# Kernel optimization log

Hardware: AMD Instinct MI355X
Metric: run time of the kernel (lower is better)

## Reference

```python
import jax, jax.numpy as jnp
import numpy as np

N_HEADS = 16

def setup_inputs() -> dict:
    key = jax.random.key(0)
    ks = jax.random.split(key, 5)
    B, T, C = 4, 2048, 1024
    x = jax.random.normal(ks[0], (B, T, C), dtype=jnp.float32)
    w_qkv = jax.random.normal(ks[1], (C, 3 * C), dtype=jnp.float32) * (C ** -0.5)
    b_qkv = jnp.zeros((3 * C,), dtype=jnp.float32)
    w_proj = jax.random.normal(ks[2], (C, C), dtype=jnp.float32) * (C ** -0.5)
    b_proj = jnp.zeros((C,), dtype=jnp.float32)
    return {"x": x, "w_qkv": w_qkv, "b_qkv": b_qkv, "w_proj": w_proj, "b_proj": b_proj}


def reference(x, w_qkv, b_qkv, w_proj, b_proj):
    B, T, C = x.shape
    H = N_HEADS
    hd = C // H
    scale = hd ** -0.5
    qkv = x @ w_qkv + b_qkv                      # [B,T,3C]
    q, k, v = jnp.split(qkv, 3, axis=-1)         # each [B,T,C]
    # -> [B,H,T,hd]
    q = q.reshape(B, T, H, hd).transpose(0, 2, 1, 3)
    k = k.reshape(B, T, H, hd).transpose(0, 2, 1, 3)
    v = v.reshape(B, T, H, hd).transpose(0, 2, 1, 3)
    attn = jnp.einsum("bhqd,bhkd->bhqk", q, k) * scale
    causal = jnp.tril(jnp.ones((T, T), dtype=bool))
    attn = jnp.where(causal, attn, -jnp.inf)
    attn = jax.nn.softmax(attn, axis=-1)         # dropout p=0 in eval/reference
    out = jnp.einsum("bhqk,bhkd->bhqd", attn, v)
    out = out.transpose(0, 2, 1, 3).reshape(B, T, C)
    return out @ w_proj + b_proj
```

## Files before the change

### kernel.cpp

```cpp
#include <hip/hip_runtime.h>
#include <hip/hip_bf16.h>


typedef float f32x4 __attribute__((ext_vector_type(4)));
typedef float f32x16 __attribute__((ext_vector_type(16)));
typedef __bf16 bf16x8 __attribute__((ext_vector_type(8)));
typedef short short8v __attribute__((ext_vector_type(8)));
typedef unsigned int u32x4 __attribute__((ext_vector_type(4)));

__device__ __forceinline__ unsigned short f2bf(float f) {
  __hip_bfloat16 h = __float2bfloat16(f);
  return __builtin_bit_cast(unsigned short, h);
}

__device__ __forceinline__ void glds16(const void* g, void* l) {
  __builtin_amdgcn_global_load_lds((const __attribute__((address_space(1))) void*)g,
                                   (__attribute__((address_space(3))) void*)l, 16, 0, 0);
}

__global__ void cvt_f32_bf16_kernel(const float* __restrict__ in,
                                    unsigned short* __restrict__ out, int n) {
  int stride = gridDim.x * blockDim.x * 4;
  for (int i = (blockIdx.x * blockDim.x + threadIdx.x) * 4; i < n; i += stride) {
    float4 v = *(const float4*)(in + i);
    ushort4 o;
    o.x = f2bf(v.x); o.y = f2bf(v.y); o.z = f2bf(v.z); o.w = f2bf(v.w);
    *(ushort4*)(out + i) = o;
  }
}

__global__ void transpose_cvt_kernel(const float* __restrict__ in,
                                     unsigned short* __restrict__ out, int K, int N) {
  __shared__ unsigned short tile[32][33];
  int tx = threadIdx.x & 31, ty = threadIdx.x >> 5;
  int n0 = blockIdx.x * 32, k0 = blockIdx.y * 32;
#pragma unroll
  for (int i = 0; i < 32; i += 8)
    tile[ty + i][tx] = f2bf(in[(size_t)(k0 + ty + i) * N + n0 + tx]);
  __syncthreads();
#pragma unroll
  for (int i = 0; i < 32; i += 8)
    out[(size_t)(n0 + ty + i) * K + k0 + tx] = tile[tx][ty + i];
}

template <int OUT_F32>
__global__ __launch_bounds__(512, 2) void gemm_bt_kernel(
    const unsigned short* __restrict__ A, const unsigned short* __restrict__ Bt,
    const float* __restrict__ bias, void* __restrict__ Cv, int M, int N, int K) {
  __shared__ unsigned short sA[3][256 * 32];
  __shared__ unsigned short sB[2][128 * 32];
  int tid = threadIdx.x;
  int lane = tid & 63, wid = tid >> 6;
  int g = lane >> 4, r16 = lane & 15;

  int gx = gridDim.x;
  int d = blockIdx.y * gx + blockIdx.x;
  int cpx = (gx * gridDim.y) >> 3;
  int nid = (d & 7) * cpx + (d >> 3);
  int m0 = (nid / gx) * 256, n0 = (nid % gx) * 128;

  int wm = wid >> 2, wn = wid & 3;
  f32x4 acc[8][2] = {};

  int srow = tid >> 2, scol = (tid & 3) * 8;
  const unsigned short* Ap0 = A + (size_t)(m0 + srow) * K + scol;
  const unsigned short* Ap1 = A + (size_t)(m0 + 128 + srow) * K + scol;
  const unsigned short* Bp = Bt + (size_t)(n0 + srow) * K + scol;

  auto STAGE_A = [&](int slot, int kt) {
    glds16(Ap0 + kt * 32, &sA[slot][tid * 8]);
    glds16(Ap1 + kt * 32, &sA[slot][4096 + tid * 8]);
  };
  auto STAGE_B = [&](int slot, int kt) {
    glds16(Bp + kt * 32, &sB[slot][tid * 8]);
  };

  int nt = K >> 5;
  STAGE_A(0, 0);
  STAGE_B(0, 0);
  STAGE_A(1, 1);
  asm volatile("s_waitcnt vmcnt(2)" ::: "memory");
  __builtin_amdgcn_s_barrier();

  int slA = 0;
#pragma unroll 1
  for (int t = 0; t < nt; ++t) {
    const unsigned short* a = sA[slA];
    const unsigned short* bb = sB[t & 1];
    bf16x8 af[4], bfr[2];
#pragma unroll
    for (int mf = 0; mf < 4; ++mf)
      af[mf] = *(const bf16x8*)&a[(wm * 128 + mf * 16 + r16) * 32 + g * 8];
#pragma unroll
    for (int nf = 0; nf < 2; ++nf)
      bfr[nf] = *(const bf16x8*)&bb[(wn * 32 + nf * 16 + r16) * 32 + g * 8];
    if (t + 1 < nt) STAGE_B((t + 1) & 1, t + 1);
    __builtin_amdgcn_s_barrier();
    __builtin_amdgcn_s_setprio(1);
#pragma unroll
    for (int mf = 0; mf < 4; ++mf)
#pragma unroll
      for (int nf = 0; nf < 2; ++nf)
        acc[mf][nf] = __builtin_amdgcn_mfma_f32_16x16x32_bf16(af[mf], bfr[nf], acc[mf][nf], 0, 0, 0);
    __builtin_amdgcn_s_setprio(0);
    bf16x8 ag[4];
#pragma unroll
    for (int mf = 0; mf < 4; ++mf)
      ag[mf] = *(const bf16x8*)&a[(wm * 128 + (mf + 4) * 16 + r16) * 32 + g * 8];
    if (t + 2 < nt) {
      int ns = slA + 2; if (ns >= 3) ns -= 3;
      STAGE_A(ns, t + 2);
      asm volatile("s_waitcnt vmcnt(2)" ::: "memory");
    } else {
      asm volatile("s_waitcnt vmcnt(0)" ::: "memory");
    }
    __builtin_amdgcn_s_barrier();
    __builtin_amdgcn_s_setprio(1);
#pragma unroll
    for (int mf = 0; mf < 4; ++mf)
#pragma unroll
      for (int nf = 0; nf < 2; ++nf)
        acc[mf + 4][nf] = __builtin_amdgcn_mfma_f32_16x16x32_bf16(ag[mf], bfr[nf], acc[mf + 4][nf], 0, 0, 0);
    __builtin_amdgcn_s_setprio(0);
    slA = slA == 2 ? 0 : slA + 1;
  }

#pragma unroll
  for (int mf = 0; mf < 8; ++mf)
#pragma unroll
    for (int nf = 0; nf < 2; ++nf)
#pragma unroll
      for (int r = 0; r < 4; ++r) {
        int row = m0 + wm * 128 + mf * 16 + g * 4 + r;
        int col = n0 + wn * 32 + nf * 16 + r16;
        float v = acc[mf][nf][r] + bias[col];
        if (OUT_F32)
          ((float*)Cv)[(size_t)row * N + col] = v;
        else
          ((unsigned short*)Cv)[(size_t)row * N + col] = f2bf(v);
      }
}

__global__ void transpose_v_kernel(const unsigned short* __restrict__ qkv,
                                   unsigned short* __restrict__ vT) {
  __shared__ unsigned short tl[64][80];
  int t0 = blockIdx.x * 64;
  int bh = blockIdx.y, b = bh >> 4, h = bh & 15;
  int tid = threadIdx.x;
  int row = tid >> 2, c0 = (tid & 3) * 16;
  const unsigned short* src =
      qkv + (size_t)(b * 2048 + t0 + row) * 3072 + 2048 + h * 64 + c0;
  short8v a0 = *(const short8v*)src;
  short8v a1 = *(const short8v*)(src + 8);
#pragma unroll
  for (int j = 0; j < 8; ++j) tl[c0 + j][row] = (unsigned short)a0[j];
#pragma unroll
  for (int j = 0; j < 8; ++j) tl[c0 + 8 + j][row] = (unsigned short)a1[j];
  __syncthreads();
  int dd = tid >> 2, tc = (tid & 3) * 16;
  unsigned short* dst = vT + (size_t)(bh * 64 + dd) * 2048 + t0 + tc;
  *(short8v*)dst = *(const short8v*)&tl[dd][tc];
  *(short8v*)(dst + 8) = *(const short8v*)&tl[dd][tc + 8];
}

__global__ __launch_bounds__(512, 4) void attn_kernel(
    const unsigned short* __restrict__ qkv, const unsigned short* __restrict__ vT,
    unsigned short* __restrict__ ao) {
  __shared__ unsigned short sK[2][4096];
  __shared__ unsigned short sV[2][4096];
  __shared__ float lbuf[8][32];
  const int T = 2048, C3 = 3072;
  const float K1 = 23.083120654223415f;
  const float K2 = 16158.66f;
  int x = blockIdx.x;
  int xcd = x & 7, rest = x >> 3;
  int bh = xcd * 8 + (rest & 7);
  int qt = 7 - (rest >> 3);
  int b = bh >> 4, h = bh & 15;
  int tid = threadIdx.x, lane = tid & 63, w = tid >> 6;
  int l31 = lane & 31, hi = lane >> 5;

  int c = tid;
  int row = c >> 3, oct = (c & 7) ^ (row & 7);
  const unsigned short* Kb = qkv + (size_t)(b * T + row) * C3 + 1024 + h * 64 + oct * 8;
  const unsigned short* Vb = vT + (size_t)(bh * 64 + row) * 2048 + oct * 8;

  auto STAGE = [&](int buf, int kt) {
    int kv0 = kt * 64;
    glds16(Kb + (size_t)kv0 * C3, &sK[buf][c * 8]);
    glds16(Vb + kv0, &sV[buf][c * 8]);
  };

  int wq0 = qt * 256 + w * 32;

  const unsigned short* qp = qkv + (size_t)(b * T + wq0 + l31) * C3 + h * 64;
  bf16x8 qf[4];
#pragma unroll
  for (int d0 = 0; d0 < 4; ++d0)
    qf[d0] = *(const bf16x8*)(qp + d0 * 16 + hi * 8);

  u32x4 onesw = {0x3F803F80u, 0x3F803F80u, 0x3F803F80u, 0x3F803F80u};
  bf16x8 vones = __builtin_bit_cast(bf16x8, onesw);

  f32x16 o[2] = {};
  f32x16 lacc = {};

  int nkv = 4 * qt + 4;
  STAGE(0, 0);
  __syncthreads();
  int cur = 0;
#pragma unroll 1
  for (int kt = 0; kt < nkv; ++kt) {
    if (kt + 1 < nkv) STAGE(cur ^ 1, kt + 1);
    int kv0 = kt * 64;
    if (kv0 <= wq0 + 31) {
      f32x16 s[2] = {};
      __builtin_amdgcn_s_setprio(1);
#pragma unroll
      for (int d0 = 0; d0 < 4; ++d0) {
        int oc = ((d0 * 2 + hi) ^ (l31 & 7)) * 8;
        bf16x8 kf0 = *(const bf16x8*)&sK[cur][l31 * 64 + oc];
        bf16x8 kf1 = *(const bf16x8*)&sK[cur][(32 + l31) * 64 + oc];
        s[0] = __builtin_amdgcn_mfma_f32_32x32x16_bf16(kf0, qf[d0], s[0], 0, 0, 0);
        s[1] = __builtin_amdgcn_mfma_f32_32x32x16_bf16(kf1, qf[d0], s[1], 0, 0, 0);
      }
      __builtin_amdgcn_s_setprio(0);

      if (kv0 + 63 > wq0) {
        int thr = wq0 + l31 - kv0 - 4 * hi;
#pragma unroll
        for (int sub = 0; sub < 2; ++sub)
#pragma unroll
          for (int r = 0; r < 16; ++r) {
            int cc = sub * 32 + (r & 3) + 8 * (r >> 2);
            s[sub][r] = (cc <= thr) ? s[sub][r] : -3e38f;
          }
      }

      int pb[2][16];
#pragma unroll
      for (int sub = 0; sub < 2; ++sub)
#pragma unroll
        for (int r = 0; r < 16; ++r)
          pb[sub][r] = (int)fmaxf(fmaf(s[sub][r], K1, K2), 0.0f);

      unsigned int pk[2][8];
#pragma unroll
      for (int sub = 0; sub < 2; ++sub)
#pragma unroll
        for (int i = 0; i < 8; ++i)
          pk[sub][i] = __builtin_amdgcn_perm((unsigned)pb[sub][2 * i + 1],
                                             (unsigned)pb[sub][2 * i], 0x05040100u);
      unsigned int rc[2][4];
#pragma unroll
      for (int sub = 0; sub < 2; ++sub) {
        unsigned int s0 = hi ? pk[sub][0] : pk[sub][2];
        unsigned int s1 = hi ? pk[sub][1] : pk[sub][3];
        unsigned int s2 = hi ? pk[sub][4] : pk[sub][6];
        unsigned int s3 = hi ? pk[sub][5] : pk[sub][7];
        rc[sub][0] = __shfl_xor(s0, 32, 64);
        rc[sub][1] = __shfl_xor(s1, 32, 64);
        rc[sub][2] = __shfl_xor(s2, 32, 64);
        rc[sub][3] = __shfl_xor(s3, 32, 64);
      }

      __builtin_amdgcn_s_setprio(1);
#pragma unroll
      for (int sub = 0; sub < 2; ++sub)
#pragma unroll
        for (int t = 0; t < 2; ++t) {
          u32x4 av;
          av.x = hi ? rc[sub][2 * t]     : pk[sub][4 * t];
          av.y = hi ? rc[sub][2 * t + 1] : pk[sub][4 * t + 1];
          av.z = hi ? pk[sub][4 * t + 2] : rc[sub][2 * t];
          av.w = hi ? pk[sub][4 * t + 3] : rc[sub][2 * t + 1];
          bf16x8 pa = __builtin_bit_cast(bf16x8, av);
          int kvs = sub * 2 + t;
          int ocv = ((kvs * 2 + hi) ^ (l31 & 7)) * 8;
          bf16x8 vf0 = *(const bf16x8*)&sV[cur][l31 * 64 + ocv];
          bf16x8 vf1 = *(const bf16x8*)&sV[cur][(32 + l31) * 64 + ocv];
          o[0] = __builtin_amdgcn_mfma_f32_32x32x16_bf16(pa, vf0, o[0], 0, 0, 0);
          o[1] = __builtin_amdgcn_mfma_f32_32x32x16_bf16(pa, vf1, o[1], 0, 0, 0);
          lacc = __builtin_amdgcn_mfma_f32_32x32x16_bf16(pa, vones, lacc, 0, 0, 0);
        }
      __builtin_amdgcn_s_setprio(0);
    }
    __syncthreads();
    cur ^= 1;
  }

  if (l31 == 0) {
#pragma unroll
    for (int r = 0; r < 16; ++r)
      lbuf[w][(r & 3) + 8 * (r >> 2) + 4 * hi] = lacc[r];
  }
  __syncthreads();
  float inv = 1.f / lbuf[w][l31];
#pragma unroll
  for (int r = 0; r < 16; ++r) {
    int qrow = (r & 3) + 8 * (r >> 2) + 4 * hi;
    float iv = __shfl(inv, qrow, 64);
    size_t base = (size_t)(b * T + wq0 + qrow) * 1024 + h * 64 + l31;
    ao[base] = f2bf(o[0][r] * iv);
    ao[base + 32] = f2bf(o[1][r] * iv);
  }
}

extern "C" void kernel_launch(void* const* d_in, const int* in_sizes, int n_in,
                              void* d_out, int out_size, void* d_ws, size_t ws_size,
                              hipStream_t stream) {
  const float* x      = (const float*)d_in[0];
  const float* w_qkv  = (const float*)d_in[1];
  const float* b_qkv  = (const float*)d_in[2];
  const float* w_proj = (const float*)d_in[3];
  const float* b_proj = (const float*)d_in[4];
  float* out = (float*)d_out;

  char* ws = (char*)d_ws;
  unsigned short* xb     = (unsigned short*)(ws);
  unsigned short* ao     = (unsigned short*)(ws);
  unsigned short* wqkvT  = (unsigned short*)(ws + (16u << 20));
  unsigned short* wprojT = (unsigned short*)(ws + (22u << 20));
  unsigned short* qkv    = (unsigned short*)(ws + (24u << 20));
  unsigned short* vT     = (unsigned short*)(ws + (72u << 20));

  cvt_f32_bf16_kernel<<<2048, 256, 0, stream>>>(x, xb, 8192 * 1024);
  transpose_cvt_kernel<<<dim3(3072 / 32, 1024 / 32), 256, 0, stream>>>(w_qkv, wqkvT, 1024, 3072);
  transpose_cvt_kernel<<<dim3(1024 / 32, 1024 / 32), 256, 0, stream>>>(w_proj, wprojT, 1024, 1024);

  gemm_bt_kernel<0><<<dim3(3072 / 128, 8192 / 256), 512, 0, stream>>>(
      xb, wqkvT, b_qkv, (void*)qkv, 8192, 3072, 1024);

  transpose_v_kernel<<<dim3(32, 64), 256, 0, stream>>>(qkv, vT);

  attn_kernel<<<dim3(512), 512, 0, stream>>>(qkv, vT, ao);

  gemm_bt_kernel<1><<<dim3(1024 / 128, 8192 / 256), 512, 0, stream>>>(
      ao, wprojT, b_proj, (void*)out, 8192, 1024, 1024);
}
```

Baseline: 175.5 us.

## Enlarge GEMM tiles to 256x256x64 with XOR-swizzled LDS and double buffering

The GEMM kernel now uses a 256x256 output tile with a K-step of 64, and each warp computes a 128x64 sub-tile (8x4 MFMA fragments). The shared-memory layout uses an XOR swizzle on 16-byte slots to avoid bank conflicts, and the old three-slot A / two-slot B split pipeline becomes plain double buffering with a full vmcnt(0) wait every iteration. This raises arithmetic intensity and halves the grid size, in exchange for 128KB of LDS (which may not fit under the 2-blocks-per-CU launch bound), more accumulator registers, and less overlap of loads with compute. The output projection grid drops to 128 blocks, which may leave CUs idle.

```diff
diff --git a/kernel.cpp b/kernel.cpp
--- a/kernel.cpp
+++ b/kernel.cpp
@@ -47,92 +47,78 @@
 __global__ __launch_bounds__(512, 2) void gemm_bt_kernel(
     const unsigned short* __restrict__ A, const unsigned short* __restrict__ Bt,
     const float* __restrict__ bias, void* __restrict__ Cv, int M, int N, int K) {
-  __shared__ unsigned short sA[3][256 * 32];
-  __shared__ unsigned short sB[2][128 * 32];
+  __shared__ unsigned short sA[2][256 * 64];
+  __shared__ unsigned short sB[2][256 * 64];
   int tid = threadIdx.x;
   int lane = tid & 63, wid = tid >> 6;
   int g = lane >> 4, r16 = lane & 15;
 
   int gx = gridDim.x;
-  int d = blockIdx.y * gx + blockIdx.x;
+  int bid = blockIdx.y * gx + blockIdx.x;
   int cpx = (gx * gridDim.y) >> 3;
-  int nid = (d & 7) * cpx + (d >> 3);
-  int m0 = (nid / gx) * 256, n0 = (nid % gx) * 128;
+  int nid = (bid & 7) * cpx + (bid >> 3);
+  int m0 = (nid / gx) * 256, n0 = (nid % gx) * 256;
 
   int wm = wid >> 2, wn = wid & 3;
-  f32x4 acc[8][2] = {};
-
-  int srow = tid >> 2, scol = (tid & 3) * 8;
-  const unsigned short* Ap0 = A + (size_t)(m0 + srow) * K + scol;
-  const unsigned short* Ap1 = A + (size_t)(m0 + 128 + srow) * K + scol;
-  const unsigned short* Bp = Bt + (size_t)(n0 + srow) * K + scol;
-
-  auto STAGE_A = [&](int slot, int kt) {
-    glds16(Ap0 + kt * 32, &sA[slot][tid * 8]);
-    glds16(Ap1 + kt * 32, &sA[slot][4096 + tid * 8]);
+  f32x4 acc[8][4] = {};
+
+  int nt = K >> 6;
+
+  auto STAGE = [&](int buf, int kt) {
+#pragma unroll
+    for (int j = 0; j < 4; ++j) {
+      int c = tid + j * 512;
+      int row = c >> 3, slot = c & 7;
+      int gcol = kt * 64 + (slot ^ (row & 7)) * 8;
+      glds16(A + (size_t)(m0 + row) * K + gcol, &sA[buf][c * 8]);
+      glds16(Bt + (size_t)(n0 + row) * K + gcol, &sB[buf][c * 8]);
+    }
   };
-  auto STAGE_B = [&](int slot, int kt) {
-    glds16(Bp + kt * 32, &sB[slot][tid * 8]);
-  };
-
-  int nt = K >> 5;
-  STAGE_A(0, 0);
-  STAGE_B(0, 0);
-  STAGE_A(1, 1);
-  asm volatile("s_waitcnt vmcnt(2)" ::: "memory");
+
+  STAGE(0, 0);
+  asm volatile("s_waitcnt vmcnt(0)" ::: "memory");
   __builtin_amdgcn_s_barrier();
 
-  int slA = 0;
+  int cur = 0;
 #pragma unroll 1
   for (int t = 0; t < nt; ++t) {
-    const unsigned short* a = sA[slA];
-    const unsigned short* bb = sB[t & 1];
-    bf16x8 af[4], bfr[2];
-#pragma unroll
-    for (int mf = 0; mf < 4; ++mf)
-      af[mf] = *(const bf16x8*)&a[(wm * 128 + mf * 16 + r16) * 32 + g * 8];
-#pragma unroll
-    for (int nf = 0; nf < 2; ++nf)
-      bfr[nf] = *(const bf16x8*)&bb[(wn * 32 + nf * 16 + r16) * 32 + g * 8];
-    if (t + 1 < nt) STAGE_B((t + 1) & 1, t + 1);
+    if (t + 1 < nt) STAGE(cur ^ 1, t + 1);
+    const unsigned short* a = sA[cur];
+    const unsigned short* bb = sB[cur];
+#pragma unroll
+    for (int kk = 0; kk < 2; ++kk) {
+      bf16x8 af[8], bf[4];
+#pragma unroll
+      for (int mf = 0; mf < 8; ++mf) {
+        int r = wm * 128 + mf * 16 + r16;
+        af[mf] = *(const bf16x8*)&a[r * 64 + (((kk * 4 + g) ^ (r & 7)) << 3)];
+      }
+#pragma unroll
+      for (int nf = 0; nf < 4; ++nf) {
+        int r = wn * 64 + nf * 16 + r16;
+        bf[nf] = *(const bf16x8*)&bb[r * 64 + (((kk * 4 + g) ^ (r & 7)) << 3)];
+      }
+      __builtin_amdgcn_s_setprio(1);
+#pragma unroll
+      for (int mf = 0; mf < 8; ++mf)
+#pragma unroll
+        for (int nf = 0; nf < 4; ++nf)
+          acc[mf][nf] = __builtin_amdgcn_mfma_f32_16x16x32_bf16(af[mf], bf[nf], acc[mf][nf], 0, 0, 0);
+      __builtin_amdgcn_s_setprio(0);
+    }
+    asm volatile("s_waitcnt vmcnt(0)" ::: "memory");
     __builtin_amdgcn_s_barrier();
-    __builtin_amdgcn_s_setprio(1);
-#pragma unroll
-    for (int mf = 0; mf < 4; ++mf)
-#pragma unroll
-      for (int nf = 0; nf < 2; ++nf)
-        acc[mf][nf] = __builtin_amdgcn_mfma_f32_16x16x32_bf16(af[mf], bfr[nf], acc[mf][nf], 0, 0, 0);
-    __builtin_amdgcn_s_setprio(0);
-    bf16x8 ag[4];
-#pragma unroll
-    for (int mf = 0; mf < 4; ++mf)
-      ag[mf] = *(const bf16x8*)&a[(wm * 128 + (mf + 4) * 16 + r16) * 32 + g * 8];
-    if (t + 2 < nt) {
-      int ns = slA + 2; if (ns >= 3) ns -= 3;
-      STAGE_A(ns, t + 2);
-      asm volatile("s_waitcnt vmcnt(2)" ::: "memory");
-    } else {
-      asm volatile("s_waitcnt vmcnt(0)" ::: "memory");
-    }
-    __builtin_amdgcn_s_barrier();
-    __builtin_amdgcn_s_setprio(1);
-#pragma unroll
-    for (int mf = 0; mf < 4; ++mf)
-#pragma unroll
-      for (int nf = 0; nf < 2; ++nf)
-        acc[mf + 4][nf] = __builtin_amdgcn_mfma_f32_16x16x32_bf16(ag[mf], bfr[nf], acc[mf + 4][nf], 0, 0, 0);
-    __builtin_amdgcn_s_setprio(0);
-    slA = slA == 2 ? 0 : slA + 1;
+    cur ^= 1;
   }
 
 #pragma unroll
   for (int mf = 0; mf < 8; ++mf)
 #pragma unroll
-    for (int nf = 0; nf < 2; ++nf)
+    for (int nf = 0; nf < 4; ++nf)
 #pragma unroll
       for (int r = 0; r < 4; ++r) {
         int row = m0 + wm * 128 + mf * 16 + g * 4 + r;
-        int col = n0 + wn * 32 + nf * 16 + r16;
+        int col = n0 + wn * 64 + nf * 16 + r16;
         float v = acc[mf][nf][r] + bias[col];
         if (OUT_F32)
           ((float*)Cv)[(size_t)row * N + col] = v;
@@ -328,13 +314,13 @@
   transpose_cvt_kernel<<<dim3(3072 / 32, 1024 / 32), 256, 0, stream>>>(w_qkv, wqkvT, 1024, 3072);
   transpose_cvt_kernel<<<dim3(1024 / 32, 1024 / 32), 256, 0, stream>>>(w_proj, wprojT, 1024, 1024);
 
-  gemm_bt_kernel<0><<<dim3(3072 / 128, 8192 / 256), 512, 0, stream>>>(
+  gemm_bt_kernel<0><<<dim3(3072 / 256, 8192 / 256), 512, 0, stream>>>(
       xb, wqkvT, b_qkv, (void*)qkv, 8192, 3072, 1024);
 
   transpose_v_kernel<<<dim3(32, 64), 256, 0, stream>>>(qkv, vT);
 
   attn_kernel<<<dim3(512), 512, 0, stream>>>(qkv, vT, ao);
 
-  gemm_bt_kernel<1><<<dim3(1024 / 128, 8192 / 256), 512, 0, stream>>>(
+  gemm_bt_kernel<1><<<dim3(1024 / 256, 8192 / 256), 512, 0, stream>>>(
       ao, wprojT, b_proj, (void*)out, 8192, 1024, 1024);
 }
```

New measurement: 191.6 us. 1.09x slower.
